# Optimization experiments

Measured on AMD Instinct MI355X. Metric: run time of the kernel, lower is better.

Reference implementation:

```python
import jax, jax.numpy as jnp
import numpy as np

B, S, D = 1, 2048, 2048
H, G = 32, 8            # n_heads, n_groups
HPG = H // G            # heads per group = 4
HD = D // H             # head_dim = 64


def setup_inputs() -> dict:
    key = jax.random.key(0)
    ks = jax.random.split(key, 5)
    w_scale = 0.02
    return {
        "x":  jax.random.normal(ks[0], (B, S, D), dtype=jnp.float32),
        "Wq": jax.random.normal(ks[1], (D, D), dtype=jnp.float32) * w_scale,
        "bq": jnp.zeros((D,), dtype=jnp.float32),
        "Wk": jax.random.normal(ks[2], (G * HD, D), dtype=jnp.float32) * w_scale,
        "bk": jnp.zeros((G * HD,), dtype=jnp.float32),
        "Wv": jax.random.normal(ks[3], (G * HD, D), dtype=jnp.float32) * w_scale,
        "bv": jnp.zeros((G * HD,), dtype=jnp.float32),
        "Wo": jax.random.normal(ks[4], (D, D), dtype=jnp.float32) * w_scale,
        "bo": jnp.zeros((D,), dtype=jnp.float32),
    }


def reference(x, Wq, bq, Wk, bk, Wv, bv, Wo, bo):
    b, n, _ = x.shape
    # projections (torch Linear: y = x @ W.T + b)
    q = x @ Wq.T + bq                              # [b, n, D]
    k = x @ Wk.T + bk                              # [b, n, G*HD]
    v = x @ Wv.T + bv                              # [b, n, G*HD]
    # q: [b, n, H, HD] -> [b, H, n, HD] -> split heads as (g h): [b, G, HPG, n, HD]
    q = q.reshape(b, n, H, HD).transpose(0, 2, 1, 3).reshape(b, G, HPG, n, HD)
    k = k.reshape(b, n, G, HD).transpose(0, 2, 1, 3)   # [b, G, n, HD]
    v = v.reshape(b, n, G, HD).transpose(0, 2, 1, 3)   # [b, G, n, HD]
    scale = 1.0 / jnp.sqrt(jnp.asarray(HD, dtype=q.dtype))
    attn_score = jnp.einsum('bghnd,bgsd->bghns', q, k) * scale
    attn_prob = jax.nn.softmax(attn_score, axis=-1)
    out = jnp.einsum('bghns,bgsd->bghnd', attn_prob, v)   # [b, G, HPG, n, HD]
    # faithful to original: rearrange 'b g h n d -> b n (h g d)' (h-major, g-minor)
    out = out.transpose(0, 3, 2, 1, 4).reshape(b, n, HPG * G * HD)
    return out @ Wo.T + bo
```

## Files before the change

### kernel.cpp

```cpp
#include <hip/hip_runtime.h>
#include <hip/hip_bf16.h>

constexpr int kS   = 2048;
constexpr int kD   = 2048;
constexpr int kG   = 8;
constexpr int kHD  = 64;
constexpr int kGHD = 512;
constexpr int kNQKV = kD + 2 * kGHD;

constexpr float kQScale = 0.125f * 1.4426950408889634f;

typedef __attribute__((ext_vector_type(8)))  _Float16 f16x8;
typedef __attribute__((ext_vector_type(4)))  float    f32x4;
typedef __attribute__((ext_vector_type(16))) float    f32x16;
typedef __attribute__((ext_vector_type(4)))  unsigned int u32x4;

__device__ __forceinline__ ushort f2h(float x) {
    return __builtin_bit_cast(ushort, (_Float16)x);
}
__device__ __forceinline__ float fast_exp2(float x) {
    return __builtin_amdgcn_exp2f(x);
}
__device__ __forceinline__ unsigned int pkrtz(float a, float b) {
    auto r = __builtin_amdgcn_cvt_pkrtz(a, b);
    return __builtin_bit_cast(unsigned int, r);
}

__global__ __launch_bounds__(256) void cvt_all(
    const float* __restrict__ x,  const float* __restrict__ Wq,
    const float* __restrict__ Wk, const float* __restrict__ Wv,
    const float* __restrict__ Wo, const float* __restrict__ bq,
    const float* __restrict__ bk, const float* __restrict__ bv,
    ushort* __restrict__ xf, ushort* __restrict__ wqkvf,
    ushort* __restrict__ wof, float* __restrict__ bqkv)
{
    constexpr size_t Nx  = (size_t)kS * kD;
    constexpr size_t NWq = (size_t)kD * kD;
    constexpr size_t NWk = (size_t)kGHD * kD;
    constexpr size_t e1 = Nx, e2 = e1 + NWq, e3 = e2 + NWk, e4 = e3 + NWk,
                     e5 = e4 + NWq;
    const size_t i = ((size_t)blockIdx.x * 256 + threadIdx.x) * 4;

    const float* src; ushort* dst; float scale = 1.f;
    if (i < e1)      { src = x  + i;        dst = xf + i; }
    else if (i < e2) { src = Wq + (i - e1); dst = wqkvf + (i - e1); scale = kQScale; }
    else if (i < e3) { src = Wk + (i - e2); dst = wqkvf + NWq + (i - e2); }
    else if (i < e4) { src = Wv + (i - e3); dst = wqkvf + NWq + NWk + (i - e3); }
    else if (i < e5) { src = Wo + (i - e4); dst = wof + (i - e4); }
    else {
        const size_t j = i - e5;
        #pragma unroll
        for (int u = 0; u < 4; ++u) {
            const size_t jj = j + u;
            if (jj < kD)              bqkv[jj] = bq[jj] * kQScale;
            else if (jj < kD + kGHD)  bqkv[jj] = bk[jj - kD];
            else if (jj < (size_t)kNQKV) bqkv[jj] = bv[jj - kD - kGHD];
        }
        return;
    }
    const float4 v = *(const float4*)src;
    ushort4 o;
    o.x = f2h(v.x * scale); o.y = f2h(v.y * scale);
    o.z = f2h(v.z * scale); o.w = f2h(v.w * scale);
    *(ushort4*)dst = o;
}

__device__ __forceinline__ int xcd_swizzle(int orig, int nwg) {
    const int cpx = nwg >> 3;
    return (orig & 7) * cpx + (orig >> 3);
}

#define GEMM_PRELUDE(Aptr, Bptr)                                              \
    const int bid  = xcd_swizzle(blockIdx.x, gridDim.x);                      \
    const int m0   = (bid / gridX) * 128;                                     \
    const int n0   = (bid % gridX) * 128;                                     \
    const int tid  = threadIdx.x;                                             \
    const int w    = tid >> 6;                                                \
    const int lane = tid & 63;                                                \
    const int wm   = w >> 2;                                                  \
    const int wn   = w & 3;                                                   \
    const int fr   = lane & 15;                                               \
    const int kq   = lane >> 4;                                               \
    const int srow = w * 16 + (lane >> 2);                                    \
    const int sslot = ((lane & 3) ^ ((lane >> 3) & 3)) * 8;                   \
    const ushort* gA = (Aptr) + (size_t)(m0 + srow) * K + sslot;              \
    const ushort* gB = (Bptr) + (size_t)(n0 + srow) * K + sslot;              \
    const int pslot = (kq ^ ((fr >> 1) & 3)) * 8;                             \
    f32x4 acc[4][2];                                                          \
    _Pragma("unroll")                                                         \
    for (int mi = 0; mi < 4; ++mi)                                            \
        _Pragma("unroll")                                                     \
        for (int ni = 0; ni < 2; ++ni) {                                      \
            f32x4 z = {0.f, 0.f, 0.f, 0.f};                                   \
            acc[mi][ni] = z;                                                  \
        }

#define GEMM_STAGE(buf, k0)                                                   \
    do {                                                                      \
        __builtin_amdgcn_global_load_lds(                                     \
            (const __attribute__((address_space(1))) void*)(gA + (k0)),       \
            (__attribute__((address_space(3))) void*)&lds[buf][0][w * 512],   \
            16, 0, 0);                                                        \
        __builtin_amdgcn_global_load_lds(                                     \
            (const __attribute__((address_space(1))) void*)(gB + (k0)),       \
            (__attribute__((address_space(3))) void*)&lds[buf][1][w * 512],   \
            16, 0, 0);                                                        \
    } while (0)

#define GEMM_KLOOP(MFMA_BODY)                                                 \
    GEMM_STAGE(0, 0);                                                         \
    __syncthreads();                                                          \
    int cur = 0;                                                              \
    for (int k0 = 0; k0 < K; k0 += 32) {                                      \
        if (k0 + 32 < K) GEMM_STAGE(cur ^ 1, k0 + 32);                        \
        f16x8 af[4], bf[2];                                                   \
        _Pragma("unroll")                                                     \
        for (int f = 0; f < 4; ++f)                                           \
            af[f] = *(const f16x8*)&lds[cur][0][(wm * 64 + f * 16 + fr) * 32 + pslot]; \
        _Pragma("unroll")                                                     \
        for (int f = 0; f < 2; ++f)                                           \
            bf[f] = *(const f16x8*)&lds[cur][1][(wn * 32 + f * 16 + fr) * 32 + pslot]; \
        __builtin_amdgcn_s_setprio(1);                                        \
        MFMA_BODY                                                             \
        __builtin_amdgcn_s_setprio(0);                                        \
        __syncthreads();                                                      \
        cur ^= 1;                                                             \
    }

__global__ __launch_bounds__(512) void gemm_qkv(
    const ushort* __restrict__ Af, const ushort* __restrict__ Bf,
    const float* __restrict__ bias,
    ushort* __restrict__ qb16, ushort* __restrict__ kb16, ushort* __restrict__ vt16,
    int K, int gridX)
{
    __shared__ ushort lds[2][2][128 * 32];

    GEMM_PRELUDE(Af, Bf)
    GEMM_KLOOP(
        _Pragma("unroll")
        for (int mi = 0; mi < 4; ++mi)
            _Pragma("unroll")
            for (int ni = 0; ni < 2; ++ni)
                acc[mi][ni] = __builtin_amdgcn_mfma_f32_16x16x32_f16(
                    af[mi], bf[ni], acc[mi][ni], 0, 0, 0);
    )

    const int seg = (n0 < kD) ? 0 : (n0 < kD + kGHD) ? 1 : 2;
    #pragma unroll
    for (int ni = 0; ni < 2; ++ni) {
        const int ncol = n0 + wn * 32 + ni * 16 + fr;
        const float bv = bias[ncol];
        #pragma unroll
        for (int mi = 0; mi < 4; ++mi) {
            #pragma unroll
            for (int i = 0; i < 4; ++i) {
                const int row = m0 + wm * 64 + mi * 16 + kq * 4 + i;
                const ushort u = f2h(acc[mi][ni][i] + bv);
                if (seg == 0)      qb16[(size_t)row * kD   + ncol]              = u;
                else if (seg == 1) kb16[(size_t)row * kGHD + (ncol - kD)]       = u;
                else               vt16[(size_t)(ncol - kD - kGHD) * kS + row]  = u;
            }
        }
    }
}

__global__ __launch_bounds__(512) void gemm_o(
    const ushort* __restrict__ Af, const ushort* __restrict__ Bf,
    const float* __restrict__ bias, float* __restrict__ C, int K, int N, int gridX)
{
    __shared__ ushort lds[2][2][128 * 32];

    GEMM_PRELUDE(Af, Bf)
    GEMM_KLOOP(
        _Pragma("unroll")
        for (int mi = 0; mi < 4; ++mi)
            _Pragma("unroll")
            for (int ni = 0; ni < 2; ++ni)
                acc[mi][ni] = __builtin_amdgcn_mfma_f32_16x16x32_f16(
                    af[mi], bf[ni], acc[mi][ni], 0, 0, 0);
    )

    #pragma unroll
    for (int ni = 0; ni < 2; ++ni) {
        const int ncol = n0 + wn * 32 + ni * 16 + fr;
        const float bv = bias[ncol];
        #pragma unroll
        for (int mi = 0; mi < 4; ++mi)
            #pragma unroll
            for (int i = 0; i < 4; ++i) {
                const int row = m0 + wm * 64 + mi * 16 + kq * 4 + i;
                C[(size_t)row * N + ncol] = acc[mi][ni][i] + bv;
            }
    }
}

__global__ __launch_bounds__(512, 4) void gqa_attn_mfma(
    const ushort* __restrict__ qb,
    const ushort* __restrict__ kb,
    const ushort* __restrict__ vt,
    ushort* __restrict__ oh)
{
    __shared__ ushort Kt[2][2][64 * 64];
    __shared__ ushort Vt[2][2][64 * 64];

    const int g    = blockIdx.y;
    const int q0   = blockIdx.x * 32;
    const int tid  = threadIdx.x;
    const int w    = tid >> 6;
    const int lane = tid & 63;
    const int hw   = w & 3;
    const int half = w >> 2;
    const int ql   = lane & 31;
    const int hi   = lane >> 5;
    const int h    = g * 4 + hw;
    const int tbase = half * (kS / 2);

    const int r0 = hw * 16 + (lane >> 3);
    const int ss = (lane & 7) ^ (r0 & 7);

#define ATTN_STAGE(buf, t)                                                         \
    do {                                                                           \
        __builtin_amdgcn_global_load_lds(                                          \
            (const __attribute__((address_space(1))) void*)                       \
                (kb + (size_t)(tbase + (t) + r0) * kGHD + g * kHD + ss * 8),       \
            (__attribute__((address_space(3))) void*)(&Kt[half][buf][(hw * 16) * 64]), \
            16, 0, 0);                                                             \
        __builtin_amdgcn_global_load_lds(                                          \
            (const __attribute__((address_space(1))) void*)                       \
                (kb + (size_t)(tbase + (t) + r0 + 8) * kGHD + g * kHD + ss * 8),   \
            (__attribute__((address_space(3))) void*)(&Kt[half][buf][(hw * 16 + 8) * 64]), \
            16, 0, 0);                                                             \
        __builtin_amdgcn_global_load_lds(                                          \
            (const __attribute__((address_space(1))) void*)                       \
                (vt + (size_t)(g * kHD + r0) * kS + tbase + (t) + ss * 8),         \
            (__attribute__((address_space(3))) void*)(&Vt[half][buf][(hw * 16) * 64]), \
            16, 0, 0);                                                             \
        __builtin_amdgcn_global_load_lds(                                          \
            (const __attribute__((address_space(1))) void*)                       \
                (vt + (size_t)(g * kHD + r0 + 8) * kS + tbase + (t) + ss * 8),     \
            (__attribute__((address_space(3))) void*)(&Vt[half][buf][(hw * 16 + 8) * 64]), \
            16, 0, 0);                                                             \
    } while (0)

    ATTN_STAGE(0, 0);

    f16x8 qf[4];
    #pragma unroll
    for (int ks = 0; ks < 4; ++ks)
        qf[ks] = *(const f16x8*)&qb[(size_t)(q0 + ql) * kD + h * kHD + ks * 16 + hi * 8];

    float mrow = -1e30f, lrow = 0.f;
    f32x16 oacc[2];
    #pragma unroll
    for (int db = 0; db < 2; ++db)
        #pragma unroll
        for (int r = 0; r < 16; ++r) oacc[db][r] = 0.f;

    int cur = 0;
    for (int t = 0; t < kS / 2; t += 64) {
        __syncthreads();

        if (t + 64 < kS / 2) ATTN_STAGE(cur ^ 1, t + 64);

        f32x16 sc[2];
        #pragma unroll
        for (int kb2 = 0; kb2 < 2; ++kb2)
            #pragma unroll
            for (int r = 0; r < 16; ++r) sc[kb2][r] = 0.f;

        {
            f16x8 kf[2][4];
            #pragma unroll
            for (int kb2 = 0; kb2 < 2; ++kb2)
                #pragma unroll
                for (int ks = 0; ks < 4; ++ks)
                    kf[kb2][ks] = *(const f16x8*)&Kt[half][cur][(kb2 * 32 + ql) * 64
                                       + (((2 * ks + hi) ^ (ql & 7)) * 8)];
            __builtin_amdgcn_s_setprio(1);
            #pragma unroll
            for (int ks = 0; ks < 4; ++ks) {
                sc[0] = __builtin_amdgcn_mfma_f32_32x32x16_f16(kf[0][ks], qf[ks], sc[0], 0, 0, 0);
                sc[1] = __builtin_amdgcn_mfma_f32_32x32x16_f16(kf[1][ks], qf[ks], sc[1], 0, 0, 0);
            }
            __builtin_amdgcn_s_setprio(0);
        }

        float mt = sc[0][0];
        #pragma unroll
        for (int kb2 = 0; kb2 < 2; ++kb2)
            #pragma unroll
            for (int r = 0; r < 16; ++r) mt = fmaxf(mt, sc[kb2][r]);
        mt = fmaxf(mt, __shfl_xor(mt, 32));

        if (__any(mt > mrow + 11.5f)) {
            const float mnew = (mt > mrow + 11.5f) ? mt : mrow;
            const float c = fast_exp2(mrow - mnew);
            lrow *= c;
            mrow = mnew;
            #pragma unroll
            for (int db = 0; db < 2; ++db)
                #pragma unroll
                for (int r = 0; r < 16; ++r) oacc[db][r] *= c;
        }

        float ps = 0.f;
        #pragma unroll
        for (int kb2 = 0; kb2 < 2; ++kb2)
            #pragma unroll
            for (int r = 0; r < 16; ++r) {
                const float p = fast_exp2(sc[kb2][r] - mrow);
                sc[kb2][r] = p;
                ps += p;
            }
        ps += __shfl_xor(ps, 32);
        lrow += ps;

        {
            f16x8 pf[2][2];
            #pragma unroll
            for (int kb2 = 0; kb2 < 2; ++kb2)
                #pragma unroll
                for (int ks = 0; ks < 2; ++ks) {
                    unsigned int a0 = pkrtz(sc[kb2][8 * ks + 0], sc[kb2][8 * ks + 1]);
                    unsigned int a1 = pkrtz(sc[kb2][8 * ks + 2], sc[kb2][8 * ks + 3]);
                    unsigned int b0 = pkrtz(sc[kb2][8 * ks + 4], sc[kb2][8 * ks + 5]);
                    unsigned int b1 = pkrtz(sc[kb2][8 * ks + 6], sc[kb2][8 * ks + 7]);
                    asm volatile("v_permlane32_swap_b32 %0, %1" : "+v"(a0), "+v"(b0));
                    asm volatile("v_permlane32_swap_b32 %0, %1" : "+v"(a1), "+v"(b1));
                    const u32x4 pu = {a0, a1, b0, b1};
                    pf[kb2][ks] = __builtin_bit_cast(f16x8, pu);
                }
            f16x8 vf[2][2][2];
            #pragma unroll
            for (int kb2 = 0; kb2 < 2; ++kb2)
                #pragma unroll
                for (int ks = 0; ks < 2; ++ks)
                    #pragma unroll
                    for (int db = 0; db < 2; ++db)
                        vf[kb2][ks][db] = *(const f16x8*)&Vt[half][cur][(db * 32 + ql) * 64
                                             + (((4 * kb2 + 2 * ks + hi) ^ (ql & 7)) * 8)];
            __builtin_amdgcn_s_setprio(1);
            #pragma unroll
            for (int kb2 = 0; kb2 < 2; ++kb2)
                #pragma unroll
                for (int ks = 0; ks < 2; ++ks)
                    #pragma unroll
                    for (int db = 0; db < 2; ++db)
                        oacc[db] = __builtin_amdgcn_mfma_f32_32x32x16_f16(
                            vf[kb2][ks][db], pf[kb2][ks], oacc[db], 0, 0, 0);
            __builtin_amdgcn_s_setprio(0);
        }
        cur ^= 1;
    }
#undef ATTN_STAGE

    __syncthreads();
    float* ox  = (float*)(&Kt[0][0][0]);
    float* mlx = (float*)(&Vt[0][0][0]);
    const int idx = hw * 64 + lane;

    if (half == 1) {
        #pragma unroll
        for (int db = 0; db < 2; ++db)
            #pragma unroll
            for (int r = 0; r < 16; ++r)
                ox[(db * 16 + r) * 256 + idx] = oacc[db][r];
        mlx[idx]       = mrow;
        mlx[256 + idx] = lrow;
    }
    __syncthreads();

    if (half == 0) {
        const float m2 = mlx[idx];
        const float l2 = mlx[256 + idx];
        const float mm = fmaxf(mrow, m2);
        const float c1 = fast_exp2(mrow - mm);
        const float c2 = fast_exp2(m2 - mm);
        const float inv = 1.f / (lrow * c1 + l2 * c2);
        const size_t rowbase = (size_t)(q0 + ql) * kD + hw * kGHD + g * kHD;
        #pragma unroll
        for (int db = 0; db < 2; ++db) {
            #pragma unroll
            for (int rr = 0; rr < 4; ++rr) {
                ushort4 o4;
                o4.x = f2h((oacc[db][rr * 4 + 0] * c1 + ox[(db * 16 + rr * 4 + 0) * 256 + idx] * c2) * inv);
                o4.y = f2h((oacc[db][rr * 4 + 1] * c1 + ox[(db * 16 + rr * 4 + 1) * 256 + idx] * c2) * inv);
                o4.z = f2h((oacc[db][rr * 4 + 2] * c1 + ox[(db * 16 + rr * 4 + 2) * 256 + idx] * c2) * inv);
                o4.w = f2h((oacc[db][rr * 4 + 3] * c1 + ox[(db * 16 + rr * 4 + 3) * 256 + idx] * c2) * inv);
                *(ushort4*)&oh[rowbase + db * 32 + rr * 8 + hi * 4] = o4;
            }
        }
    }
}

extern "C" void kernel_launch(void* const* d_in, const int* in_sizes, int n_in,
                              void* d_out, int out_size, void* d_ws, size_t ws_size,
                              hipStream_t stream)
{
    const float* x  = (const float*)d_in[0];
    const float* Wq = (const float*)d_in[1];
    const float* bq = (const float*)d_in[2];
    const float* Wk = (const float*)d_in[3];
    const float* bk = (const float*)d_in[4];
    const float* Wv = (const float*)d_in[5];
    const float* bv = (const float*)d_in[6];
    const float* Wo = (const float*)d_in[7];
    const float* bo = (const float*)d_in[8];
    float* out = (float*)d_out;

    char* p = (char*)d_ws;
    ushort* xf    = (ushort*)p; p += (size_t)kS * kD * 2;
    ushort* wqkvf = (ushort*)p; p += (size_t)kNQKV * kD * 2;
    ushort* wof   = (ushort*)p; p += (size_t)kD * kD * 2;
    float*  bqkv  = (float*)p;  p += 16384;
    ushort* qb16  = (ushort*)p; p += (size_t)kS * kD * 2;
    ushort* kb16  = (ushort*)p; p += (size_t)kS * kGHD * 2;
    ushort* vt16  = (ushort*)p; p += (size_t)kGHD * kS * 2;
    ushort* aoh   = (ushort*)p;

    constexpr size_t kCvtElems = (size_t)kS * kD + 2 * (size_t)kD * kD
                               + 2 * (size_t)kGHD * kD + kNQKV;
    cvt_all<<<(kCvtElems + 1023) / 1024, 256, 0, stream>>>(
        x, Wq, Wk, Wv, Wo, bq, bk, bv, xf, wqkvf, wof, bqkv);

    gemm_qkv<<<(kNQKV / 128) * (kS / 128), 512, 0, stream>>>(
        xf, wqkvf, bqkv, qb16, kb16, vt16, kD, kNQKV / 128);

    gqa_attn_mfma<<<dim3(kS / 32, kG), 512, 0, stream>>>(qb16, kb16, vt16, aoh);

    gemm_o<<<(kD / 128) * (kS / 128), 512, 0, stream>>>(
        aoh, wof, bo, out, kD, kD, kD / 128);
}
```

Baseline: 141.0 us.

## Use split-K across warp halves with 64-wide K tiles in GEMMs

Both projection GEMMs now stage 64-wide K slices per iteration, and each half of the eight waves handles half of every slice (split-K within the block). Each wave owns a 64x64 output sub-tile with 16 accumulators instead of 8, which halves the number of loop iterations and barriers and raises MFMA work per LDS fragment load. The two halves' partial sums are reduced through LDS before the epilogue. In exchange the kernel uses twice the LDS, more registers per wave, and an extra LDS reduction step, and only half the waves write output.

Measured after the change: 134.7 us. 4.4% less time.

```diff
diff --git a/kernel.cpp b/kernel.cpp
--- a/kernel.cpp
+++ b/kernel.cpp
@@ -77,120 +77,145 @@
     const int tid  = threadIdx.x;                                             \
     const int w    = tid >> 6;                                                \
     const int lane = tid & 63;                                                \
-    const int wm   = w >> 2;                                                  \
-    const int wn   = w & 3;                                                   \
+    const int kph  = w >> 2;                                                  \
+    const int wm   = (w & 3) >> 1;                                            \
+    const int wn   = w & 1;                                                   \
     const int fr   = lane & 15;                                               \
     const int kq   = lane >> 4;                                               \
-    const int srow = w * 16 + (lane >> 2);                                    \
-    const int sslot = ((lane & 3) ^ ((lane >> 3) & 3)) * 8;                   \
+    const int srow = w * 16 + (lane >> 3);                                    \
+    const int sslot = ((lane & 7) ^ (lane >> 3)) * 8;                         \
     const ushort* gA = (Aptr) + (size_t)(m0 + srow) * K + sslot;              \
     const ushort* gB = (Bptr) + (size_t)(n0 + srow) * K + sslot;              \
-    const int pslot = (kq ^ ((fr >> 1) & 3)) * 8;                             \
-    f32x4 acc[4][2];                                                          \
+    f32x4 acc[4][4];                                                          \
     _Pragma("unroll")                                                         \
     for (int mi = 0; mi < 4; ++mi)                                            \
         _Pragma("unroll")                                                     \
-        for (int ni = 0; ni < 2; ++ni) {                                      \
+        for (int ni = 0; ni < 4; ++ni) {                                      \
             f32x4 z = {0.f, 0.f, 0.f, 0.f};                                   \
             acc[mi][ni] = z;                                                  \
         }
 
 #define GEMM_STAGE(buf, k0)                                                   \
     do {                                                                      \
-        __builtin_amdgcn_global_load_lds(                                     \
-            (const __attribute__((address_space(1))) void*)(gA + (k0)),       \
-            (__attribute__((address_space(3))) void*)&lds[buf][0][w * 512],   \
-            16, 0, 0);                                                        \
-        __builtin_amdgcn_global_load_lds(                                     \
-            (const __attribute__((address_space(1))) void*)(gB + (k0)),       \
-            (__attribute__((address_space(3))) void*)&lds[buf][1][w * 512],   \
-            16, 0, 0);                                                        \
+        _Pragma("unroll")                                                     \
+        for (int j = 0; j < 2; ++j) {                                         \
+            __builtin_amdgcn_global_load_lds(                                 \
+                (const __attribute__((address_space(1))) void*)               \
+                    (gA + (size_t)j * 8 * K + (k0)),                          \
+                (__attribute__((address_space(3))) void*)                    \
+                    &lds[buf][0][(w * 16 + j * 8) * 64],                      \
+                16, 0, 0);                                                    \
+            __builtin_amdgcn_global_load_lds(                                 \
+                (const __attribute__((address_space(1))) void*)               \
+                    (gB + (size_t)j * 8 * K + (k0)),                          \
+                (__attribute__((address_space(3))) void*)                    \
+                    &lds[buf][1][(w * 16 + j * 8) * 64],                      \
+                16, 0, 0);                                                    \
+        }                                                                     \
     } while (0)
 
-#define GEMM_KLOOP(MFMA_BODY)                                                 \
+#define GEMM_KLOOP                                                            \
     GEMM_STAGE(0, 0);                                                         \
     __syncthreads();                                                          \
     int cur = 0;                                                              \
-    for (int k0 = 0; k0 < K; k0 += 32) {                                      \
-        if (k0 + 32 < K) GEMM_STAGE(cur ^ 1, k0 + 32);                        \
-        f16x8 af[4], bf[2];                                                   \
-        _Pragma("unroll")                                                     \
-        for (int f = 0; f < 4; ++f)                                           \
-            af[f] = *(const f16x8*)&lds[cur][0][(wm * 64 + f * 16 + fr) * 32 + pslot]; \
-        _Pragma("unroll")                                                     \
-        for (int f = 0; f < 2; ++f)                                           \
-            bf[f] = *(const f16x8*)&lds[cur][1][(wn * 32 + f * 16 + fr) * 32 + pslot]; \
+    for (int k0 = 0; k0 < K; k0 += 64) {                                      \
+        if (k0 + 64 < K) GEMM_STAGE(cur ^ 1, k0 + 64);                        \
+        f16x8 af[4], bf[4];                                                   \
+        _Pragma("unroll")                                                     \
+        for (int f = 0; f < 4; ++f) {                                         \
+            const int ra = wm * 64 + f * 16 + fr;                             \
+            const int rb = wn * 64 + f * 16 + fr;                             \
+            af[f] = *(const f16x8*)&lds[cur][0][ra * 64                       \
+                        + (((kph * 4 + kq) ^ (ra & 7)) * 8)];                 \
+            bf[f] = *(const f16x8*)&lds[cur][1][rb * 64                       \
+                        + (((kph * 4 + kq) ^ (rb & 7)) * 8)];                 \
+        }                                                                     \
         __builtin_amdgcn_s_setprio(1);                                        \
-        MFMA_BODY                                                             \
+        _Pragma("unroll")                                                     \
+        for (int mi = 0; mi < 4; ++mi)                                        \
+            _Pragma("unroll")                                                 \
+            for (int ni = 0; ni < 4; ++ni)                                    \
+                acc[mi][ni] = __builtin_amdgcn_mfma_f32_16x16x32_f16(         \
+                    af[mi], bf[ni], acc[mi][ni], 0, 0, 0);                    \
         __builtin_amdgcn_s_setprio(0);                                        \
         __syncthreads();                                                      \
         cur ^= 1;                                                             \
     }
 
-__global__ __launch_bounds__(512) void gemm_qkv(
+#define GEMM_MERGE                                                            \
+    float* mlds = (float*)&lds[0][0][0];                                      \
+    if (w >= 4) {                                                             \
+        _Pragma("unroll")                                                     \
+        for (int c = 0; c < 16; ++c)                                          \
+            *(f32x4*)&mlds[(w - 4) * 4096 + c * 256 + lane * 4]               \
+                = acc[c >> 2][c & 3];                                         \
+    }                                                                         \
+    __syncthreads();                                                          \
+    if (w < 4) {                                                              \
+        _Pragma("unroll")                                                     \
+        for (int c = 0; c < 16; ++c) {                                        \
+            const f32x4 part = *(const f32x4*)&mlds[w * 4096 + c * 256        \
+                                                    + lane * 4];              \
+            acc[c >> 2][c & 3] += part;                                       \
+        }                                                                     \
+    }
+
+__global__ __launch_bounds__(512, 4) void gemm_qkv(
     const ushort* __restrict__ Af, const ushort* __restrict__ Bf,
     const float* __restrict__ bias,
     ushort* __restrict__ qb16, ushort* __restrict__ kb16, ushort* __restrict__ vt16,
     int K, int gridX)
 {
-    __shared__ ushort lds[2][2][128 * 32];
+    __shared__ ushort lds[2][2][128 * 64];
 
     GEMM_PRELUDE(Af, Bf)
-    GEMM_KLOOP(
-        _Pragma("unroll")
-        for (int mi = 0; mi < 4; ++mi)
-            _Pragma("unroll")
-            for (int ni = 0; ni < 2; ++ni)
-                acc[mi][ni] = __builtin_amdgcn_mfma_f32_16x16x32_f16(
-                    af[mi], bf[ni], acc[mi][ni], 0, 0, 0);
-    )
-
-    const int seg = (n0 < kD) ? 0 : (n0 < kD + kGHD) ? 1 : 2;
-    #pragma unroll
-    for (int ni = 0; ni < 2; ++ni) {
-        const int ncol = n0 + wn * 32 + ni * 16 + fr;
-        const float bv = bias[ncol];
-        #pragma unroll
-        for (int mi = 0; mi < 4; ++mi) {
-            #pragma unroll
-            for (int i = 0; i < 4; ++i) {
-                const int row = m0 + wm * 64 + mi * 16 + kq * 4 + i;
-                const ushort u = f2h(acc[mi][ni][i] + bv);
-                if (seg == 0)      qb16[(size_t)row * kD   + ncol]              = u;
-                else if (seg == 1) kb16[(size_t)row * kGHD + (ncol - kD)]       = u;
-                else               vt16[(size_t)(ncol - kD - kGHD) * kS + row]  = u;
+    GEMM_KLOOP
+    GEMM_MERGE
+
+    if (w < 4) {
+        const int seg = (n0 < kD) ? 0 : (n0 < kD + kGHD) ? 1 : 2;
+        #pragma unroll
+        for (int ni = 0; ni < 4; ++ni) {
+            const int ncol = n0 + wn * 64 + ni * 16 + fr;
+            const float bv = bias[ncol];
+            #pragma unroll
+            for (int mi = 0; mi < 4; ++mi) {
+                #pragma unroll
+                for (int i = 0; i < 4; ++i) {
+                    const int row = m0 + wm * 64 + mi * 16 + kq * 4 + i;
+                    const ushort u = f2h(acc[mi][ni][i] + bv);
+                    if (seg == 0)      qb16[(size_t)row * kD   + ncol]              = u;
+                    else if (seg == 1) kb16[(size_t)row * kGHD + (ncol - kD)]       = u;
+                    else               vt16[(size_t)(ncol - kD - kGHD) * kS + row]  = u;
+                }
             }
         }
     }
 }
 
-__global__ __launch_bounds__(512) void gemm_o(
+__global__ __launch_bounds__(512, 4) void gemm_o(
     const ushort* __restrict__ Af, const ushort* __restrict__ Bf,
     const float* __restrict__ bias, float* __restrict__ C, int K, int N, int gridX)
 {
-    __shared__ ushort lds[2][2][128 * 32];
+    __shared__ ushort lds[2][2][128 * 64];
 
     GEMM_PRELUDE(Af, Bf)
-    GEMM_KLOOP(
-        _Pragma("unroll")
-        for (int mi = 0; mi < 4; ++mi)
-            _Pragma("unroll")
-            for (int ni = 0; ni < 2; ++ni)
-                acc[mi][ni] = __builtin_amdgcn_mfma_f32_16x16x32_f16(
-                    af[mi], bf[ni], acc[mi][ni], 0, 0, 0);
-    )
-
-    #pragma unroll
-    for (int ni = 0; ni < 2; ++ni) {
-        const int ncol = n0 + wn * 32 + ni * 16 + fr;
-        const float bv = bias[ncol];
-        #pragma unroll
-        for (int mi = 0; mi < 4; ++mi)
-            #pragma unroll
-            for (int i = 0; i < 4; ++i) {
-                const int row = m0 + wm * 64 + mi * 16 + kq * 4 + i;
-                C[(size_t)row * N + ncol] = acc[mi][ni][i] + bv;
-            }
+    GEMM_KLOOP
+    GEMM_MERGE
+
+    if (w < 4) {
+        #pragma unroll
+        for (int ni = 0; ni < 4; ++ni) {
+            const int ncol = n0 + wn * 64 + ni * 16 + fr;
+            const float bv = bias[ncol];
+            #pragma unroll
+            for (int mi = 0; mi < 4; ++mi)
+                #pragma unroll
+                for (int i = 0; i < 4; ++i) {
+                    const int row = m0 + wm * 64 + mi * 16 + kq * 4 + i;
+                    C[(size_t)row * N + ncol] = acc[mi][ni][i] + bv;
+                }
+        }
     }
 }
 
```
